# Kernel optimization log

Hardware: AMD Instinct MI355X
Metric: run time of the kernel (lower is better)

Reference implementation:

```python
import jax, jax.numpy as jnp
import numpy as np

B, PP, LP, H = 128, 1024, 128, 256  # graphs, protein atoms/graph, ligand atoms/graph, hidden
NP, NL = B * PP, B * LP


def setup_inputs() -> dict:
    key = jax.random.key(0)
    ks = jax.random.split(key, 16)
    s = 0.02
    return {
        "protein_pos": 10.0 * jax.random.normal(ks[0], (NP, 3), jnp.float32),
        "ligand_pos": 10.0 * jax.random.normal(ks[1], (NL, 3), jnp.float32),
        "protein_element": jax.random.randint(ks[2], (NP,), 0, 128),
        "protein_aa": jax.random.randint(ks[3], (NP,), 0, 32),
        "protein_is_backbone": jax.random.randint(ks[4], (NP,), 0, 2),
        "ligand_type": jax.random.randint(ks[5], (NL,), 0, 16),
        "protein_batch": jnp.repeat(jnp.arange(B), PP),  # block-contiguous segments
        "ligand_batch": jnp.repeat(jnp.arange(B), LP),
        "E_elem": s * jax.random.normal(ks[6], (128, H), jnp.float32),
        "E_aa": s * jax.random.normal(ks[7], (32, H), jnp.float32),
        "E_bb": s * jax.random.normal(ks[8], (2, H), jnp.float32),
        "E_lig": s * jax.random.normal(ks[9], (16, H), jnp.float32),
        "Wd1": s * jax.random.normal(ks[10], (H, H), jnp.float32),
        "bd1": jnp.zeros((H,), jnp.float32),
        "Wd2": s * jax.random.normal(ks[11], (H, H), jnp.float32),
        "bd2": jnp.zeros((H,), jnp.float32),
        "Wa1": s * jax.random.normal(ks[12], (2 * H + 2, H), jnp.float32),
        "ba1": jnp.zeros((H,), jnp.float32),
        "Wa2": s * jax.random.normal(ks[13], (H, 1), jnp.float32),
        "ba2": jnp.zeros((1,), jnp.float32),
    }


def _pool_by_batch(x, batch, bsz):
    # mean-pool rows of x into bsz segments (index_add_ + bincount in torch)
    summed = jax.ops.segment_sum(x, batch, num_segments=bsz)
    counts = jax.ops.segment_sum(jnp.ones((x.shape[0],), x.dtype), batch, num_segments=bsz)
    return summed / jnp.maximum(counts, 1.0)[:, None]


def reference(protein_pos, ligand_pos, protein_element, protein_aa, protein_is_backbone,
              ligand_type, protein_batch, ligand_batch,
              E_elem, E_aa, E_bb, E_lig, Wd1, bd1, Wd2, bd2, Wa1, ba1, Wa2, ba2):
    # protein / ligand node embeddings
    h_protein = E_elem[protein_element] + E_aa[protein_aa] + E_bb[protein_is_backbone]
    h_ligand = E_lig[ligand_type]

    # compose_context: protein first, then ligand (mask_ligand = [0]*NP + [1]*NL)
    h_ctx = jnp.concatenate([h_protein, h_ligand], axis=0)

    # stub denoiser: pointwise 2-layer SiLU MLP producing out['h']
    h_out = jax.nn.silu(h_ctx @ Wd1 + bd1) @ Wd2 + bd2
    protein_h = h_out[:protein_pos.shape[0]]
    ligand_h = h_out[protein_pos.shape[0]:]

    pooled_protein = _pool_by_batch(protein_h, protein_batch, B)  # [B, H]
    pooled_ligand = _pool_by_batch(ligand_h, ligand_batch, B)     # [B, H]

    # contact features: per-graph cdist(lig, prot), min over protein atoms,
    # then mean & min over ligand atoms. Uniform block layout -> dense reshape.
    prot = protein_pos.reshape(B, PP, 3)
    lig = ligand_pos.reshape(B, LP, 3)
    d2 = jnp.sum((lig[:, :, None, :] - prot[:, None, :, :]) ** 2, axis=-1)  # [B, LP, PP]
    dist = jnp.sqrt(d2)
    min_lp = dist.min(axis=2)                                    # [B, LP]
    contact = jnp.stack([min_lp.mean(axis=1), min_lp.min(axis=1)], axis=-1)  # [B, 2]

    graph_feat = jnp.concatenate([pooled_protein, pooled_ligand, contact], axis=-1)  # [B, 2H+2]
    affinity = (jax.nn.silu(graph_feat @ Wa1 + ba1) @ Wa2 + ba2).squeeze(-1)  # [B]
    return affinity
```

## Files before the change

### kernel.cpp

```cpp
#include <hip/hip_runtime.h>
#include <hip/hip_bf16.h>

typedef _Float16 f16;
typedef _Float16 h4 __attribute__((ext_vector_type(4)));
typedef float f32x4 __attribute__((ext_vector_type(4)));

#define B_   128
#define PP_  1024
#define LP_  128
#define H_   256
#define NP_  131072
#define NL_  16384


__global__ void __launch_bounds__(256) tbl_k(
    const float* __restrict__ W1,
    const float* __restrict__ Ee, const float* __restrict__ Ea,
    const float* __restrict__ Eb, const float* __restrict__ El,
    const float* __restrict__ bd1,
    f16* __restrict__ tbl, float* __restrict__ ysum, float* __restrict__ out)
{
  __shared__ float s0[256], s1[256];
  const int bid = blockIdx.x, tid = threadIdx.x;
  ysum[bid * 256 + tid] = 0.f;
  if (bid == 90 && tid < 128) out[tid] = 0.f;
  if (bid >= 89) return;

  const int r0 = bid * 2;
  const float* s;
  float badd = 0.f;
  if (r0 < 128)      s = Ee + r0 * 256;
  else if (r0 < 160) s = Ea + (r0 - 128) * 256;
  else if (r0 < 162) { s = Eb + (r0 - 160) * 256; badd = bd1[tid]; }
  else               { s = El + (r0 - 162) * 256; badd = bd1[tid]; }
  s0[tid] = s[tid];
  s1[tid] = s[256 + tid];
  __syncthreads();
  float a0 = 0.f, a1 = 0.f, b0 = 0.f, b1 = 0.f;
#pragma unroll 4
  for (int k = 0; k < 256; k += 2) {
    const float w0 = W1[(k)     * 256 + tid];
    const float w1 = W1[(k + 1) * 256 + tid];
    a0 += s0[k] * w0;     b0 += s0[k + 1] * w1;
    a1 += s1[k] * w0;     b1 += s1[k + 1] * w1;
  }
  tbl[r0 * 256 + tid]       = (f16)(a0 + b0 + badd);
  tbl[(r0 + 1) * 256 + tid] = (f16)(a1 + b1 + badd);
}

__global__ void __launch_bounds__(256, 4) mid_k(
    const float* __restrict__ W2, const float* __restrict__ Wa1,
    const float* __restrict__ ba1, const float* __restrict__ bd2,
    const float* __restrict__ ppos, const float* __restrict__ lpos,
    const int* __restrict__ pel, const int* __restrict__ paa,
    const int* __restrict__ pbb, const int* __restrict__ ltyp,
    const f16* __restrict__ tbl,
    float* __restrict__ wc, float* __restrict__ cvec,
    float* __restrict__ gmin, float* __restrict__ ysum)
{
  __shared__ __align__(16) float sm[2048];
  const int bid = blockIdx.x, tid = threadIdx.x;

  if (bid < 64) {
    const int half = bid >> 5, r0 = (bid & 31) * 8;
#pragma unroll
    for (int r = 0; r < 8; ++r) sm[r * 256 + tid] = W2[(r0 + r) * 256 + tid];
    __syncthreads();
    const float* W = Wa1 + half * 65536 + tid;
    float a[8];
#pragma unroll
    for (int r = 0; r < 8; ++r) a[r] = 0.f;
#pragma unroll 4
    for (int n = 0; n < 256; ++n) {
      const float w = W[n * 256];
#pragma unroll
      for (int r = 0; r < 8; ++r) a[r] += sm[r * 256 + n] * w;
    }
    const float scale = half ? (1.f / (float)LP_) : (1.f / (float)PP_);
#pragma unroll
    for (int r = 0; r < 8; ++r)
      wc[half * 65536 + (r0 + r) * 256 + tid] = a[r] * scale;

  } else if (bid == 64) {
    float a = ba1[tid];
#pragma unroll 8
    for (int n = 0; n < 256; ++n)
      a += bd2[n] * (Wa1[n * 256 + tid] + Wa1[(256 + n) * 256 + tid]);
    cvec[tid] = a;

  } else if (bid < 321) {
    const int cb = bid - 65, b = cb >> 1, half = cb & 1;
    float* px = sm;
    float* py = sm + 512;
    float* pz = sm + 1024;
#pragma unroll
    for (int r = 0; r < 2; ++r) {
      const int i = r * 256 + tid;
      const float* p = ppos + ((size_t)b * PP_ + half * 512 + i) * 3;
      px[i] = p[0]; py[i] = p[1]; pz[i] = p[2];
    }
    __syncthreads();
    const int lig = tid >> 1, part = tid & 1;
    const float* lp = lpos + ((size_t)b * LP_ + lig) * 3;
    const float lx = lp[0], ly = lp[1], lz = lp[2];
    const float4* X4 = (const float4*)(px + part * 256);
    const float4* Y4 = (const float4*)(py + part * 256);
    const float4* Z4 = (const float4*)(pz + part * 256);
    float m = 3.4e38f;
#pragma unroll 4
    for (int i = 0; i < 64; ++i) {
      float4 X = X4[i], Y = Y4[i], Z = Z4[i];
      float dx, dy, dz, d2;
      dx = lx - X.x; dy = ly - Y.x; dz = lz - Z.x;
      d2 = dx * dx + dy * dy + dz * dz; m = fminf(m, d2);
      dx = lx - X.y; dy = ly - Y.y; dz = lz - Z.y;
      d2 = dx * dx + dy * dy + dz * dz; m = fminf(m, d2);
      dx = lx - X.z; dy = ly - Y.z; dz = lz - Z.z;
      d2 = dx * dx + dy * dy + dz * dz; m = fminf(m, d2);
      dx = lx - X.w; dy = ly - Y.w; dz = lz - Z.w;
      d2 = dx * dx + dy * dy + dz * dz; m = fminf(m, d2);
    }
    m = fminf(m, __shfl_xor(m, 1));
    if (!part) gmin[cb * 128 + lig] = m;

  } else {
    const int idx = bid - 321;
    const int batch = idx / 18, g = idx % 18;
    const int wave = tid >> 6, lane = tid & 63;
    const int c0 = lane * 4;
    f32x4 acc = (f32x4){0.f, 0.f, 0.f, 0.f};

    if (g < 16) {
      const int base = batch * PP_ + g * 64 + wave * 16;
#pragma unroll 4
      for (int r = 0; r < 16; ++r) {
        const int i = base + r;
        h4 va = *(const h4*)(tbl + pel[i] * 256 + c0);
        h4 vb = *(const h4*)(tbl + 32768 + paa[i] * 256 + c0);
        h4 vc = *(const h4*)(tbl + 40960 + pbb[i] * 256 + c0);
#pragma unroll
        for (int k = 0; k < 4; ++k) {
          float pre = (float)va[k] + (float)vb[k] + (float)vc[k];
          acc[k] += pre * __builtin_amdgcn_rcpf(1.f + __expf(-pre));
        }
      }
    } else {
      const int base = batch * LP_ + (g - 16) * 64 + wave * 16;
#pragma unroll 4
      for (int r = 0; r < 16; ++r) {
        const int i = base + r;
        h4 v = *(const h4*)(tbl + 41472 + ltyp[i] * 256 + c0);
#pragma unroll
        for (int k = 0; k < 4; ++k) {
          float pre = (float)v[k];
          acc[k] += pre * __builtin_amdgcn_rcpf(1.f + __expf(-pre));
        }
      }
    }

    f32x4* red = (f32x4*)sm;
    if (wave) red[(wave - 1) * 64 + lane] = acc;
    __syncthreads();
    if (wave == 0) {
      f32x4 a1 = red[lane], a2 = red[64 + lane], a3 = red[128 + lane];
      float* pool = ysum + (g < 16 ? 0 : 32768) + batch * 256 + c0;
#pragma unroll
      for (int k = 0; k < 4; ++k)
        atomicAdd(pool + k, ((acc[k] + a1[k]) + (a2[k] + a3[k])));
    }
  }
}

__global__ void __launch_bounds__(256) head_k(
    const float* __restrict__ ysum, const float* __restrict__ wc,
    const float* __restrict__ cvec, const float* __restrict__ Wa1,
    const float* __restrict__ Wa2, const float* __restrict__ ba2,
    const float* __restrict__ gmin, float* __restrict__ out)
{
  __shared__ float ysc[512];
  __shared__ float part[256];
  __shared__ float lmin[128];
  __shared__ float cls[2];
  __shared__ float red[2];
  const int b = blockIdx.x >> 1, jh = blockIdx.x & 1, tid = threadIdx.x;

  ysc[tid]       = ysum[b * 256 + tid];
  ysc[256 + tid] = ysum[32768 + b * 256 + tid];
  if (tid < 128) {
    const float m = fminf(gmin[(b * 2) * 128 + tid], gmin[(b * 2 + 1) * 128 + tid]);
    lmin[tid] = sqrtf(m);
  }
  __syncthreads();

  if (tid < 64) {
    const float a0 = lmin[tid], a1 = lmin[tid + 64];
    float sm = a0 + a1, mn = fminf(a0, a1);
#pragma unroll
    for (int off = 32; off; off >>= 1) {
      sm += __shfl_down(sm, off);
      mn = fminf(mn, __shfl_down(mn, off));
    }
    if (tid == 0) { cls[0] = sm * (1.f / (float)LP_); cls[1] = mn; }
  }

  {
    const int kh = tid >> 7, jj = tid & 127;
    const float* W = wc + kh * 65536 + jh * 128 + jj;
    const float* ys = ysc + kh * 256;
    float a[8];
#pragma unroll
    for (int u = 0; u < 8; ++u) a[u] = 0.f;
#pragma unroll 2
    for (int k = 0; k < 256; k += 8) {
#pragma unroll
      for (int u = 0; u < 8; ++u)
        a[u] += ys[k + u] * W[(k + u) * 256];
    }
    part[tid] = ((a[0] + a[1]) + (a[2] + a[3])) + ((a[4] + a[5]) + (a[6] + a[7]));
  }
  __syncthreads();

  if (tid < 128) {
    const int j = jh * 128 + tid;
    float pre = part[tid] + part[128 + tid] + cvec[j]
              + cls[0] * Wa1[512 * 256 + j] + cls[1] * Wa1[513 * 256 + j];
    float si = pre * __builtin_amdgcn_rcpf(1.f + __expf(-pre));
    float p = si * Wa2[j];
#pragma unroll
    for (int off = 32; off; off >>= 1) p += __shfl_down(p, off);
    if ((tid & 63) == 0) red[tid >> 6] = p;
  }
  __syncthreads();
  if (tid == 0) atomicAdd(out + b, red[0] + red[1] + (jh ? 0.f : ba2[0]));
}

extern "C" void kernel_launch(void* const* d_in, const int* in_sizes, int n_in,
                              void* d_out, int out_size, void* d_ws, size_t ws_size,
                              hipStream_t stream)
{
  const float* protein_pos = (const float*)d_in[0];
  const float* ligand_pos  = (const float*)d_in[1];
  const int*   pel  = (const int*)d_in[2];
  const int*   paa  = (const int*)d_in[3];
  const int*   pbb  = (const int*)d_in[4];
  const int*   ltyp = (const int*)d_in[5];
  const float* Ee  = (const float*)d_in[8];
  const float* Ea  = (const float*)d_in[9];
  const float* Eb  = (const float*)d_in[10];
  const float* El  = (const float*)d_in[11];
  const float* Wd1 = (const float*)d_in[12];
  const float* bd1 = (const float*)d_in[13];
  const float* Wd2 = (const float*)d_in[14];
  const float* bd2 = (const float*)d_in[15];
  const float* Wa1 = (const float*)d_in[16];
  const float* ba1 = (const float*)d_in[17];
  const float* Wa2 = (const float*)d_in[18];
  const float* ba2 = (const float*)d_in[19];
  float* out = (float*)d_out;

  char* ws = (char*)d_ws;
  f16*   tbl  = (f16*)(ws);
  float* ysum = (float*)(ws + 98304);
  float* wc   = (float*)(ws + 360448);
  float* cvec = (float*)(ws + 884736);
  float* gmin = (float*)(ws + 885760);

  tbl_k<<<256, 256, 0, stream>>>(Wd1, Ee, Ea, Eb, El, bd1, tbl, ysum, out);
  mid_k<<<2625, 256, 0, stream>>>(Wd2, Wa1, ba1, bd2, protein_pos, ligand_pos,
                                  pel, paa, pbb, ltyp, tbl, wc, cvec, gmin, ysum);
  head_k<<<256, 256, 0, stream>>>(ysum, wc, cvec, Wa1, Wa2, ba2, gmin, out);
}
```

Baseline: 133.7 us.

## Merge three kernels into two with last-block-done head fusion

Measured after the change: 212.8 us. 1.59x slower.

```diff
diff --git a/kernel.cpp b/kernel.cpp
--- a/kernel.cpp
+++ b/kernel.cpp
@@ -13,56 +13,49 @@
 #define NL_  16384
 
 
-__global__ void __launch_bounds__(256) tbl_k(
+__global__ void __launch_bounds__(256) prep_k(
     const float* __restrict__ W1,
     const float* __restrict__ Ee, const float* __restrict__ Ea,
     const float* __restrict__ Eb, const float* __restrict__ El,
     const float* __restrict__ bd1,
-    f16* __restrict__ tbl, float* __restrict__ ysum, float* __restrict__ out)
-{
-  __shared__ float s0[256], s1[256];
-  const int bid = blockIdx.x, tid = threadIdx.x;
-  ysum[bid * 256 + tid] = 0.f;
-  if (bid == 90 && tid < 128) out[tid] = 0.f;
-  if (bid >= 89) return;
-
-  const int r0 = bid * 2;
-  const float* s;
-  float badd = 0.f;
-  if (r0 < 128)      s = Ee + r0 * 256;
-  else if (r0 < 160) s = Ea + (r0 - 128) * 256;
-  else if (r0 < 162) { s = Eb + (r0 - 160) * 256; badd = bd1[tid]; }
-  else               { s = El + (r0 - 162) * 256; badd = bd1[tid]; }
-  s0[tid] = s[tid];
-  s1[tid] = s[256 + tid];
-  __syncthreads();
-  float a0 = 0.f, a1 = 0.f, b0 = 0.f, b1 = 0.f;
-#pragma unroll 4
-  for (int k = 0; k < 256; k += 2) {
-    const float w0 = W1[(k)     * 256 + tid];
-    const float w1 = W1[(k + 1) * 256 + tid];
-    a0 += s0[k] * w0;     b0 += s0[k + 1] * w1;
-    a1 += s1[k] * w0;     b1 += s1[k + 1] * w1;
-  }
-  tbl[r0 * 256 + tid]       = (f16)(a0 + b0 + badd);
-  tbl[(r0 + 1) * 256 + tid] = (f16)(a1 + b1 + badd);
-}
-
-__global__ void __launch_bounds__(256, 4) mid_k(
     const float* __restrict__ W2, const float* __restrict__ Wa1,
     const float* __restrict__ ba1, const float* __restrict__ bd2,
     const float* __restrict__ ppos, const float* __restrict__ lpos,
-    const int* __restrict__ pel, const int* __restrict__ paa,
-    const int* __restrict__ pbb, const int* __restrict__ ltyp,
-    const f16* __restrict__ tbl,
-    float* __restrict__ wc, float* __restrict__ cvec,
-    float* __restrict__ gmin, float* __restrict__ ysum)
+    f16* __restrict__ tbl, float* __restrict__ wc, float* __restrict__ cvec,
+    float* __restrict__ gmin, float* __restrict__ ysum,
+    unsigned* __restrict__ cnt)
 {
   __shared__ __align__(16) float sm[2048];
   const int bid = blockIdx.x, tid = threadIdx.x;
-
-  if (bid < 64) {
-    const int half = bid >> 5, r0 = (bid & 31) * 8;
+  if (bid < 256) ysum[bid * 256 + tid] = 0.f;
+
+  if (bid < 89) {
+    const int r0 = bid * 2;
+    const float* s;
+    float badd = 0.f;
+    if (r0 < 128)      s = Ee + r0 * 256;
+    else if (r0 < 160) s = Ea + (r0 - 128) * 256;
+    else if (r0 < 162) { s = Eb + (r0 - 160) * 256; badd = bd1[tid]; }
+    else               { s = El + (r0 - 162) * 256; badd = bd1[tid]; }
+    float* s0 = sm;
+    float* s1 = sm + 256;
+    s0[tid] = s[tid];
+    s1[tid] = s[256 + tid];
+    __syncthreads();
+    float a0 = 0.f, a1 = 0.f, b0 = 0.f, b1 = 0.f;
+#pragma unroll 4
+    for (int k = 0; k < 256; k += 2) {
+      const float w0 = W1[(k)     * 256 + tid];
+      const float w1 = W1[(k + 1) * 256 + tid];
+      a0 += s0[k] * w0;     b0 += s0[k + 1] * w1;
+      a1 += s1[k] * w0;     b1 += s1[k + 1] * w1;
+    }
+    tbl[r0 * 256 + tid]       = (f16)(a0 + b0 + badd);
+    tbl[(r0 + 1) * 256 + tid] = (f16)(a1 + b1 + badd);
+
+  } else if (bid < 153) {
+    const int idx = bid - 89;
+    const int half = idx >> 5, r0 = (idx & 31) * 8;
 #pragma unroll
     for (int r = 0; r < 8; ++r) sm[r * 256 + tid] = W2[(r0 + r) * 256 + tid];
     __syncthreads();
@@ -81,15 +74,18 @@
     for (int r = 0; r < 8; ++r)
       wc[half * 65536 + (r0 + r) * 256 + tid] = a[r] * scale;
 
-  } else if (bid == 64) {
+  } else if (bid == 153) {
     float a = ba1[tid];
 #pragma unroll 8
     for (int n = 0; n < 256; ++n)
       a += bd2[n] * (Wa1[n * 256 + tid] + Wa1[(256 + n) * 256 + tid]);
     cvec[tid] = a;
 
-  } else if (bid < 321) {
-    const int cb = bid - 65, b = cb >> 1, half = cb & 1;
+  } else if (bid == 154) {
+    if (tid < 128) cnt[tid] = 0u;
+
+  } else if (bid >= 256) {
+    const int cb = bid - 256, b = cb >> 1, half = cb & 1;
     float* px = sm;
     float* py = sm + 512;
     float* pz = sm + 1024;
@@ -122,42 +118,55 @@
     }
     m = fminf(m, __shfl_xor(m, 1));
     if (!part) gmin[cb * 128 + lig] = m;
-
+  }
+}
+
+__global__ void __launch_bounds__(256, 4) main_k(
+    const int* __restrict__ pel, const int* __restrict__ paa,
+    const int* __restrict__ pbb, const int* __restrict__ ltyp,
+    const f16* __restrict__ tbl, const float* __restrict__ wc,
+    const float* __restrict__ cvec, const float* __restrict__ Wa1,
+    const float* __restrict__ Wa2, const float* __restrict__ ba2,
+    const float* __restrict__ gmin, float* __restrict__ ysum,
+    unsigned* __restrict__ cnt, float* __restrict__ out)
+{
+  __shared__ __align__(16) float sm[2048];
+  __shared__ unsigned finfl;
+  const int bid = blockIdx.x, tid = threadIdx.x;
+  const int batch = bid / 18, g = bid % 18;
+  const int wave = tid >> 6, lane = tid & 63;
+  const int c0 = lane * 4;
+  f32x4 acc = (f32x4){0.f, 0.f, 0.f, 0.f};
+
+  if (g < 16) {
+    const int base = batch * PP_ + g * 64 + wave * 16;
+#pragma unroll 4
+    for (int r = 0; r < 16; ++r) {
+      const int i = base + r;
+      h4 va = *(const h4*)(tbl + pel[i] * 256 + c0);
+      h4 vb = *(const h4*)(tbl + 32768 + paa[i] * 256 + c0);
+      h4 vc = *(const h4*)(tbl + 40960 + pbb[i] * 256 + c0);
+#pragma unroll
+      for (int k = 0; k < 4; ++k) {
+        float pre = (float)va[k] + (float)vb[k] + (float)vc[k];
+        acc[k] += pre * __builtin_amdgcn_rcpf(1.f + __expf(-pre));
+      }
+    }
   } else {
-    const int idx = bid - 321;
-    const int batch = idx / 18, g = idx % 18;
-    const int wave = tid >> 6, lane = tid & 63;
-    const int c0 = lane * 4;
-    f32x4 acc = (f32x4){0.f, 0.f, 0.f, 0.f};
-
-    if (g < 16) {
-      const int base = batch * PP_ + g * 64 + wave * 16;
-#pragma unroll 4
-      for (int r = 0; r < 16; ++r) {
-        const int i = base + r;
-        h4 va = *(const h4*)(tbl + pel[i] * 256 + c0);
-        h4 vb = *(const h4*)(tbl + 32768 + paa[i] * 256 + c0);
-        h4 vc = *(const h4*)(tbl + 40960 + pbb[i] * 256 + c0);
-#pragma unroll
-        for (int k = 0; k < 4; ++k) {
-          float pre = (float)va[k] + (float)vb[k] + (float)vc[k];
-          acc[k] += pre * __builtin_amdgcn_rcpf(1.f + __expf(-pre));
-        }
+    const int base = batch * LP_ + (g - 16) * 64 + wave * 16;
+#pragma unroll 4
+    for (int r = 0; r < 16; ++r) {
+      const int i = base + r;
+      h4 v = *(const h4*)(tbl + 41472 + ltyp[i] * 256 + c0);
+#pragma unroll
+      for (int k = 0; k < 4; ++k) {
+        float pre = (float)v[k];
+        acc[k] += pre * __builtin_amdgcn_rcpf(1.f + __expf(-pre));
       }
-    } else {
-      const int base = batch * LP_ + (g - 16) * 64 + wave * 16;
-#pragma unroll 4
-      for (int r = 0; r < 16; ++r) {
-        const int i = base + r;
-        h4 v = *(const h4*)(tbl + 41472 + ltyp[i] * 256 + c0);
-#pragma unroll
-        for (int k = 0; k < 4; ++k) {
-          float pre = (float)v[k];
-          acc[k] += pre * __builtin_amdgcn_rcpf(1.f + __expf(-pre));
-        }
-      }
-    }
-
+    }
+  }
+
+  {
     f32x4* red = (f32x4*)sm;
     if (wave) red[(wave - 1) * 64 + lane] = acc;
     __syncthreads();
@@ -169,69 +178,72 @@
         atomicAdd(pool + k, ((acc[k] + a1[k]) + (a2[k] + a3[k])));
     }
   }
-}
-
-__global__ void __launch_bounds__(256) head_k(
-    const float* __restrict__ ysum, const float* __restrict__ wc,
-    const float* __restrict__ cvec, const float* __restrict__ Wa1,
-    const float* __restrict__ Wa2, const float* __restrict__ ba2,
-    const float* __restrict__ gmin, float* __restrict__ out)
-{
-  __shared__ float ysc[512];
-  __shared__ float part[256];
-  __shared__ float lmin[128];
-  __shared__ float cls[2];
-  __shared__ float red[2];
-  const int b = blockIdx.x >> 1, jh = blockIdx.x & 1, tid = threadIdx.x;
-
-  ysc[tid]       = ysum[b * 256 + tid];
-  ysc[256 + tid] = ysum[32768 + b * 256 + tid];
+
+  __syncthreads();
+  if (tid == 0) {
+    __threadfence();
+    finfl = (atomicAdd(cnt + batch, 1u) == 17u) ? 1u : 0u;
+  }
+  __syncthreads();
+  if (!finfl) return;
+  __threadfence();
+
+  float* ysc  = sm;
+  float* part = sm + 512;
+  float* lmin = sm + 1536;
+  float* cls  = sm + 1664;
+  float* red2 = sm + 1668;
+
+  ysc[tid]       = ysum[batch * 256 + tid];
+  ysc[256 + tid] = ysum[32768 + batch * 256 + tid];
   if (tid < 128) {
-    const float m = fminf(gmin[(b * 2) * 128 + tid], gmin[(b * 2 + 1) * 128 + tid]);
+    const float m = fminf(gmin[(batch * 2) * 128 + tid],
+                          gmin[(batch * 2 + 1) * 128 + tid]);
     lmin[tid] = sqrtf(m);
   }
   __syncthreads();
 
   if (tid < 64) {
     const float a0 = lmin[tid], a1 = lmin[tid + 64];
-    float sm = a0 + a1, mn = fminf(a0, a1);
+    float s = a0 + a1, mn = fminf(a0, a1);
 #pragma unroll
     for (int off = 32; off; off >>= 1) {
-      sm += __shfl_down(sm, off);
+      s += __shfl_down(s, off);
       mn = fminf(mn, __shfl_down(mn, off));
     }
-    if (tid == 0) { cls[0] = sm * (1.f / (float)LP_); cls[1] = mn; }
+    if (tid == 0) { cls[0] = s * (1.f / (float)LP_); cls[1] = mn; }
   }
 
   {
-    const int kh = tid >> 7, jj = tid & 127;
-    const float* W = wc + kh * 65536 + jh * 128 + jj;
-    const float* ys = ysc + kh * 256;
-    float a[8];
-#pragma unroll
-    for (int u = 0; u < 8; ++u) a[u] = 0.f;
-#pragma unroll 2
-    for (int k = 0; k < 256; k += 8) {
-#pragma unroll
-      for (int u = 0; u < 8; ++u)
-        a[u] += ys[k + u] * W[(k + u) * 256];
-    }
-    part[tid] = ((a[0] + a[1]) + (a[2] + a[3])) + ((a[4] + a[5]) + (a[6] + a[7]));
-  }
-  __syncthreads();
-
-  if (tid < 128) {
-    const int j = jh * 128 + tid;
-    float pre = part[tid] + part[128 + tid] + cvec[j]
+    const int jq = tid & 63, kc = tid >> 6;
+    const int j0 = jq * 4;
+    const float* W = wc + kc * 32768 + j0;
+    const float* ys = ysc + kc * 128;
+    f32x4 a4 = (f32x4){0.f, 0.f, 0.f, 0.f};
+#pragma unroll 8
+    for (int k = 0; k < 128; ++k) {
+      const float y = ys[k];
+      const f32x4 w = *(const f32x4*)(W + k * 256);
+      a4 += y * w;
+    }
+    ((f32x4*)part)[kc * 64 + jq] = a4;
+  }
+  __syncthreads();
+
+  {
+    const int j = tid;
+    float pre = ((part[j] + part[256 + j]) + (part[512 + j] + part[768 + j]))
+              + cvec[j]
               + cls[0] * Wa1[512 * 256 + j] + cls[1] * Wa1[513 * 256 + j];
     float si = pre * __builtin_amdgcn_rcpf(1.f + __expf(-pre));
     float p = si * Wa2[j];
 #pragma unroll
     for (int off = 32; off; off >>= 1) p += __shfl_down(p, off);
-    if ((tid & 63) == 0) red[tid >> 6] = p;
-  }
-  __syncthreads();
-  if (tid == 0) atomicAdd(out + b, red[0] + red[1] + (jh ? 0.f : ba2[0]));
+    if ((tid & 63) == 0) red2[tid >> 6] = p;
+  }
+  __syncthreads();
+  if (tid == 0)
+    out[batch] = ((red2[0] + red2[1]) + (red2[2] + red2[3])) + ba2[0];
 }
 
 extern "C" void kernel_launch(void* const* d_in, const int* in_sizes, int n_in,
@@ -259,14 +271,16 @@
   float* out = (float*)d_out;
 
   char* ws = (char*)d_ws;
-  f16*   tbl  = (f16*)(ws);
-  float* ysum = (float*)(ws + 98304);
-  float* wc   = (float*)(ws + 360448);
-  float* cvec = (float*)(ws + 884736);
-  float* gmin = (float*)(ws + 885760);
-
-  tbl_k<<<256, 256, 0, stream>>>(Wd1, Ee, Ea, Eb, El, bd1, tbl, ysum, out);
-  mid_k<<<2625, 256, 0, stream>>>(Wd2, Wa1, ba1, bd2, protein_pos, ligand_pos,
-                                  pel, paa, pbb, ltyp, tbl, wc, cvec, gmin, ysum);
-  head_k<<<256, 256, 0, stream>>>(ysum, wc, cvec, Wa1, Wa2, ba2, gmin, out);
+  f16*      tbl  = (f16*)(ws);
+  float*    ysum = (float*)(ws + 98304);
+  float*    wc   = (float*)(ws + 360448);
+  float*    cvec = (float*)(ws + 884736);
+  float*    gmin = (float*)(ws + 885760);
+  unsigned* cnt  = (unsigned*)(ws + 1016832);
+
+  prep_k<<<512, 256, 0, stream>>>(Wd1, Ee, Ea, Eb, El, bd1, Wd2, Wa1, ba1, bd2,
+                                  protein_pos, ligand_pos,
+                                  tbl, wc, cvec, gmin, ysum, cnt);
+  main_k<<<B_ * 18, 256, 0, stream>>>(pel, paa, pbb, ltyp, tbl, wc, cvec,
+                                      Wa1, Wa2, ba2, gmin, ysum, cnt, out);
 }
```
